# Kernel tuning notes

Measured on AMD Instinct MI355X. Metric: run time of the kernel, lower is better.

## Reference

```python
import jax, jax.numpy as jnp
import numpy as np

N_NODES = 20000
N_EDGES = 640000
D_IN = 128
D_OUT = 128


def setup_inputs() -> dict:
    key = jax.random.key(0)
    k1, k2, k3, k4 = jax.random.split(key, 4)
    x = jax.random.normal(k1, (N_NODES, D_IN), dtype=jnp.float32)
    edge_index = jax.random.randint(k2, (2, N_EDGES), 0, N_NODES, dtype=jnp.int64)
    edge_weight = jnp.ones((N_EDGES,), dtype=jnp.float32)
    # Linear(in_feats, out_feats) params (PyTorch convention: W [out, in])
    bound = 1.0 / np.sqrt(D_IN)
    W = jax.random.uniform(k3, (D_OUT, D_IN), minval=-bound, maxval=bound, dtype=jnp.float32)
    b = jax.random.uniform(k4, (D_OUT,), minval=-bound, maxval=bound, dtype=jnp.float32)
    return {"x": x, "edge_index": edge_index, "edge_weight": edge_weight, "W": W, "b": b}


def reference(x, edge_index, edge_weight, W, b):
    # MeanAggregator: h = Linear(x); out = row-normalized spmm(adj, h)
    h = x @ W.T + b  # [N, D_OUT]
    row, col = edge_index[0], edge_index[1]
    # message = w_ij * h[j], scattered into row i  (spmm with COO adjacency)
    msg = h[col] * edge_weight[:, None]  # [E, D_OUT]
    agg = jax.ops.segment_sum(msg, row, num_segments=N_NODES)  # [N, D_OUT]
    deg = jax.ops.segment_sum(edge_weight, row, num_segments=N_NODES)  # [N]
    deg_inv = jnp.where(deg > 0, 1.0 / deg, 0.0)
    out = agg * deg_inv[:, None]
    # normalize=True -> F.normalize(out, p=2, dim=-1)
    norm = jnp.linalg.norm(out, axis=-1, keepdims=True)
    out = out / jnp.maximum(norm, 1e-12)
    return out
```

## Files before the change

kernel.cpp:

```cpp
#include <hip/hip_runtime.h>
#include <hip/hip_bf16.h>
#include <math.h>

#define N_NODES 20000
#define N_EDGES 640000
#define D 128

#define BSHIFT 4
#define BNODES 16
#define NB 1250
#define CAP2 768
#define AGG_T 1024
#define NBLK1 160
#define CHUNK 4000
#define GPAD 16
#define CASTBLK 625

#define GROWS 16

typedef __attribute__((ext_vector_type(8))) short bf16x8;
typedef __attribute__((ext_vector_type(4))) float f32x4;

static __device__ __forceinline__ unsigned short f2bf(float f) {
  unsigned u = __float_as_uint(f);
  return (unsigned short)((u + 0x7fffu + ((u >> 16) & 1u)) >> 16);
}
static __device__ __forceinline__ float bflo(unsigned v) {
  return __uint_as_float(v << 16);
}
static __device__ __forceinline__ float bfhi(unsigned v) {
  return __uint_as_float(v & 0xffff0000u);
}

__global__ __launch_bounds__(256) void zero_kernel(int* __restrict__ p, int n) {
  const int i = blockIdx.x * 256 + threadIdx.x;
  if (i < n) p[i] = 0;
}

__global__ __launch_bounds__(AGG_T) void castbin_kernel(
    const float* __restrict__ x, const float* __restrict__ W,
    const int* __restrict__ rows, const int* __restrict__ cols,
    const float* __restrict__ ew,
    unsigned* __restrict__ xb, unsigned* __restrict__ Wb,
    int* __restrict__ gcur, uint2* __restrict__ bins) {
  __shared__ uint2 stage[CHUNK];
  __shared__ int cnt[NB];
  __shared__ int lbase[NB];
  __shared__ int gbase[NB];
  const int tid = threadIdx.x;
  if (blockIdx.x < NBLK1) {
    const int e0 = blockIdx.x * CHUNK;
    for (int i = tid; i < NB; i += AGG_T) cnt[i] = 0;
    __syncthreads();
    const int4* r4 = reinterpret_cast<const int4*>(rows + e0);
    int4 rv;
    const bool own = tid < CHUNK / 4;
    if (own) {
      rv = r4[tid];
      atomicAdd(&cnt[rv.x >> BSHIFT], 1);
      atomicAdd(&cnt[rv.y >> BSHIFT], 1);
      atomicAdd(&cnt[rv.z >> BSHIFT], 1);
      atomicAdd(&cnt[rv.w >> BSHIFT], 1);
    }
    __syncthreads();
    if (tid < 64) {
      int carry = 0;
      for (int c0 = 0; c0 < NB; c0 += 64) {
        const int idx = c0 + tid;
        const int v = (idx < NB) ? cnt[idx] : 0;
        int s = v;
#pragma unroll
        for (int off = 1; off < 64; off <<= 1) {
          const int t = __shfl_up(s, off);
          if (tid >= off) s += t;
        }
        if (idx < NB) lbase[idx] = carry + s - v;
        carry += __shfl(s, 63);
      }
    }
    for (int i = tid; i < NB; i += AGG_T) {
      const int c = cnt[i];
      gbase[i] = c ? atomicAdd(&gcur[i * GPAD], c) : 0;
    }
    __syncthreads();
    for (int i = tid; i < NB; i += AGG_T) cnt[i] = 0;
    __syncthreads();
    if (own) {
      const int4 cv = reinterpret_cast<const int4*>(cols + e0)[tid];
      const float4 wv = reinterpret_cast<const float4*>(ew + e0)[tid];
      const int rr[4] = {rv.x, rv.y, rv.z, rv.w};
      const int cc[4] = {cv.x, cv.y, cv.z, cv.w};
      const float ww[4] = {wv.x, wv.y, wv.z, wv.w};
#pragma unroll
      for (int u = 0; u < 4; ++u) {
        const int b = rr[u] >> BSHIFT;
        const int r = atomicAdd(&cnt[b], 1);
        stage[lbase[b] + r] =
            make_uint2(((unsigned)rr[u] << 16) | (unsigned)cc[u],
                       __float_as_uint(ww[u]));
      }
    }
    __syncthreads();
    for (int i = tid; i < CHUNK; i += AGG_T) {
      const uint2 e = stage[i];
      const int b = (int)(e.x >> 20);
      const int p = gbase[b] + (i - lbase[b]);
      if (p < CAP2) bins[(size_t)b * CAP2 + p] = e;
    }
  } else {
    const int i = (blockIdx.x - NBLK1) * AGG_T + tid;
    {
      const float4 v = *reinterpret_cast<const float4*>(&x[(size_t)i * 4]);
      uint2 o;
      o.x = (unsigned)f2bf(v.x) | ((unsigned)f2bf(v.y) << 16);
      o.y = (unsigned)f2bf(v.z) | ((unsigned)f2bf(v.w) << 16);
      *reinterpret_cast<uint2*>(&xb[(size_t)i * 2]) = o;
    }
    if (i < D * D / 4) {
      const float4 v = *reinterpret_cast<const float4*>(&W[(size_t)i * 4]);
      uint2 o;
      o.x = (unsigned)f2bf(v.x) | ((unsigned)f2bf(v.y) << 16);
      o.y = (unsigned)f2bf(v.z) | ((unsigned)f2bf(v.w) << 16);
      *reinterpret_cast<uint2*>(&Wb[(size_t)i * 2]) = o;
    }
  }
}

__global__ __launch_bounds__(AGG_T) void agg_gemm_kernel(
    const unsigned* __restrict__ xb, const int* __restrict__ gcur,
    const uint2* __restrict__ bins, const unsigned* __restrict__ Wb,
    const float* __restrict__ bias, float* __restrict__ out) {
  __shared__ uint2 list[CAP2];
  __shared__ unsigned aggls[BNODES * 64];
  __shared__ int cnt[BNODES];
  __shared__ int base[BNODES];
  __shared__ float degls[BNODES];
  const int b = blockIdx.x;
  const int tid = threadIdx.x;
  const int n = min(gcur[b * GPAD], CAP2);
  if (tid < BNODES) cnt[tid] = 0;
  __syncthreads();

  uint2 ev;
  int rk = -1, rl = 0;
  if (tid < n) {
    ev = bins[(size_t)b * CAP2 + tid];
    rl = (int)(ev.x >> 16) & 15;
    rk = atomicAdd(&cnt[rl], 1);
  }
  __syncthreads();
  if (tid < 64) {
    const int c = (tid < BNODES) ? cnt[tid] : 0;
    int s = c;
#pragma unroll
    for (int off = 1; off < BNODES; off <<= 1) {
      const int t = __shfl_up(s, off);
      if (tid >= off) s += t;
    }
    if (tid < BNODES) base[tid] = s - c;
  }
  __syncthreads();
  if (rk >= 0) list[base[rl] + rk] = ev;
  __syncthreads();

  const int wv = tid >> 6, lane = tid & 63;
  const int q4 = lane >> 4, fidx = lane & 15;
  {
    const int s = base[wv];
    const int ke = s + cnt[wv];
    float a[8] = {0.f, 0.f, 0.f, 0.f, 0.f, 0.f, 0.f, 0.f};
    float dw = 0.f;
    for (int k = s; k < ke; k += 32) {
      uint4 v[8];
      float w[8];
#pragma unroll
      for (int u = 0; u < 8; ++u) {
        int idx = k + u * 4 + q4;
        const bool ok = idx < ke;
        if (!ok) idx = ke - 1;
        const uint2 e = list[idx];
        w[u] = ok ? __uint_as_float(e.y) : 0.f;
        v[u] = *reinterpret_cast<const uint4*>(
            &xb[(size_t)(e.x & 0xffffu) * (D / 2) + fidx * 4]);
      }
#pragma unroll
      for (int u = 0; u < 8; ++u) {
        a[0] += bflo(v[u].x) * w[u]; a[1] += bfhi(v[u].x) * w[u];
        a[2] += bflo(v[u].y) * w[u]; a[3] += bfhi(v[u].y) * w[u];
        a[4] += bflo(v[u].z) * w[u]; a[5] += bfhi(v[u].z) * w[u];
        a[6] += bflo(v[u].w) * w[u]; a[7] += bfhi(v[u].w) * w[u];
        dw += w[u];
      }
    }
#pragma unroll
    for (int j = 0; j < 8; ++j) {
      a[j] += __shfl_xor(a[j], 16);
      a[j] += __shfl_xor(a[j], 32);
    }
    dw += __shfl_xor(dw, 16);
    dw += __shfl_xor(dw, 32);
    const float dinv = dw > 0.f ? 1.f / dw : 0.f;
    if (lane == 0) degls[wv] = dw;
    if (q4 == 0) {
      uint4 o;
      o.x = (unsigned)f2bf(a[0] * dinv) | ((unsigned)f2bf(a[1] * dinv) << 16);
      o.y = (unsigned)f2bf(a[2] * dinv) | ((unsigned)f2bf(a[3] * dinv) << 16);
      o.z = (unsigned)f2bf(a[4] * dinv) | ((unsigned)f2bf(a[5] * dinv) << 16);
      o.w = (unsigned)f2bf(a[6] * dinv) | ((unsigned)f2bf(a[7] * dinv) << 16);
      *reinterpret_cast<uint4*>(
          &aggls[wv * 64 + ((fidx * 4) ^ ((wv & 7) << 2))]) = o;
    }
  }
  __syncthreads();

  if (wv != 0) return;
  const int arow = lane & 15;
  const int koff = (lane >> 4) * 4;

  bf16x8 afr[4];
#pragma unroll
  for (int kk = 0; kk < 4; ++kk) {
    const int wbase = (kk * 16 + koff) ^ ((arow & 7) << 2);
    union { uint4 u; bf16x8 v; } cv;
    cv.u = *reinterpret_cast<const uint4*>(&aggls[arow * 64 + wbase]);
    afr[kk] = cv.v;
  }

  f32x4 acc[8];
#pragma unroll
  for (int t = 0; t < 8; ++t) {
    const int o = t * 16 + (lane & 15);
    f32x4 c = {0.f, 0.f, 0.f, 0.f};
#pragma unroll
    for (int kk = 0; kk < 4; ++kk) {
      union { uint4 u; bf16x8 v; } cv;
      cv.u = *reinterpret_cast<const uint4*>(
          &Wb[(size_t)o * (D / 2) + kk * 16 + koff]);
      c = __builtin_amdgcn_mfma_f32_16x16x32_bf16(afr[kk], cv.v, c, 0, 0, 0);
    }
    acc[t] = c;
  }

  float ss[4] = {0.f, 0.f, 0.f, 0.f};
#pragma unroll
  for (int t = 0; t < 8; ++t) {
    const float bc = bias[t * 16 + (lane & 15)];
#pragma unroll
    for (int r = 0; r < 4; ++r) {
      const float y = acc[t][r] + bc;
      acc[t][r] = y;
      ss[r] += y * y;
    }
  }
#pragma unroll
  for (int r = 0; r < 4; ++r) {
#pragma unroll
    for (int off = 1; off < 16; off <<= 1)
      ss[r] += __shfl_xor(ss[r], off);
  }
  const int row0 = b * BNODES;
  float scale[4];
#pragma unroll
  for (int r = 0; r < 4; ++r) {
    const int lrow = (lane >> 4) * 4 + r;
    const float dw = degls[lrow];
    scale[r] = (dw > 0.f) ? 1.f / fmaxf(sqrtf(ss[r]), 1e-12f) : 0.f;
  }
#pragma unroll
  for (int t = 0; t < 8; ++t) {
#pragma unroll
    for (int r = 0; r < 4; ++r) {
      const int lrow = (lane >> 4) * 4 + r;
      out[(size_t)(row0 + lrow) * D + t * 16 + (lane & 15)] =
          acc[t][r] * scale[r];
    }
  }
}

__global__ __launch_bounds__(256) void scatter_kernel(
    const float* __restrict__ x, const int* __restrict__ rows,
    const int* __restrict__ cols, const float* __restrict__ ew,
    float* __restrict__ out, float* __restrict__ degw) {
  const int e = blockIdx.x * 4 + (threadIdx.x >> 6);
  const int lane = threadIdx.x & 63;
  if (e >= N_EDGES) return;
  const int r = rows[e];
  const int c = cols[e];
  const float w = ew[e];
  const float2 v = *reinterpret_cast<const float2*>(&x[(size_t)c * D + lane * 2]);
  atomicAdd(&out[(size_t)r * D + lane * 2], v.x * w);
  atomicAdd(&out[(size_t)r * D + lane * 2 + 1], v.y * w);
  if (lane == 0) atomicAdd(&degw[r], w);
}

__global__ __launch_bounds__(256) void linear_norm_kernel(
    const float* __restrict__ W, const float* __restrict__ b,
    const float* __restrict__ degw, float* __restrict__ out) {
  __shared__ float Ws[D][D + 1];
  __shared__ float xs[GROWS][D];
  __shared__ float dws[GROWS];
  const int tid = threadIdx.x;
  const int row0 = blockIdx.x * GROWS;
  for (int idx = tid; idx < D * D; idx += 256)
    Ws[idx >> 7][idx & 127] = W[idx];
  if (tid < GROWS) dws[tid] = degw[row0 + tid];
  __syncthreads();
  for (int idx = tid; idx < GROWS * D; idx += 256) {
    const int r = idx >> 7;
    const float dw = dws[r];
    const float dinv = dw > 0.f ? 1.f / dw : 0.f;
    xs[r][idx & 127] = out[(size_t)(row0 + r) * D + (idx & 127)] * dinv;
  }
  __syncthreads();
  const int o = tid & 127;
  const int rh = tid >> 7;
  float acc[GROWS / 2];
#pragma unroll
  for (int j = 0; j < GROWS / 2; ++j) acc[j] = 0.f;
  for (int k = 0; k < D; ++k) {
    const float wv = Ws[o][k];
#pragma unroll
    for (int j = 0; j < GROWS / 2; ++j)
      acc[j] += xs[rh + 2 * j][k] * wv;
  }
  const float bias = b[o];
  __syncthreads();
#pragma unroll
  for (int j = 0; j < GROWS / 2; ++j)
    xs[rh + 2 * j][o] = acc[j] + bias;
  __syncthreads();
  const int w = tid >> 6, lane = tid & 63;
#pragma unroll
  for (int q = 0; q < 4; ++q) {
    const int r = w * 4 + q;
    const float2 v = *reinterpret_cast<const float2*>(&xs[r][lane * 2]);
    float ss = v.x * v.x + v.y * v.y;
#pragma unroll
    for (int off = 1; off < 64; off <<= 1) ss += __shfl_xor(ss, off);
    const float dw = dws[r];
    const float scale = (dw > 0.f) ? 1.f / fmaxf(sqrtf(ss), 1e-12f) : 0.f;
    *reinterpret_cast<float2*>(&out[(size_t)(row0 + r) * D + lane * 2]) =
        make_float2(v.x * scale, v.y * scale);
  }
}

extern "C" void kernel_launch(void* const* d_in, const int* in_sizes, int n_in,
                              void* d_out, int out_size, void* d_ws, size_t ws_size,
                              hipStream_t stream) {
  const float* x  = (const float*)d_in[0];
  const int*   ei = (const int*)d_in[1];
  const float* ew = (const float*)d_in[2];
  const float* W  = (const float*)d_in[3];
  const float* b  = (const float*)d_in[4];
  float* out = (float*)d_out;
  char* ws = (char*)d_ws;

  const int* rows = ei;
  const int* cols = ei + N_EDGES;

  size_t off = 0;
  int* gcur = (int*)(ws + off);        off += (size_t)NB * GPAD * 4;
  float* degw = (float*)(ws + off);    off += (size_t)N_NODES * 4;
  unsigned* xb = (unsigned*)(ws + off);  off += (size_t)N_NODES * (D / 2) * 4;
  unsigned* Wb = (unsigned*)(ws + off);  off += (size_t)D * (D / 2) * 4;
  uint2* bins = (uint2*)(ws + off);    off += (size_t)NB * CAP2 * 8;
  const size_t main_bytes = off;
  const size_t fallback_bytes = (size_t)NB * GPAD * 4 + (size_t)N_NODES * 4;

  if (ws_size >= main_bytes) {
    zero_kernel<<<(NB * GPAD + 255) / 256, 256, 0, stream>>>(gcur, NB * GPAD);
    castbin_kernel<<<NBLK1 + CASTBLK, AGG_T, 0, stream>>>(x, W, rows, cols, ew,
                                                          xb, Wb, gcur, bins);
    agg_gemm_kernel<<<NB, AGG_T, 0, stream>>>(xb, gcur, bins, Wb, b, out);
  } else if (ws_size >= fallback_bytes) {
    hipMemsetAsync(out, 0, (size_t)N_NODES * D * 4, stream);
    hipMemsetAsync(degw, 0, (size_t)N_NODES * 4, stream);
    scatter_kernel<<<(N_EDGES + 3) / 4, 256, 0, stream>>>(x, rows, cols, ew, out, degw);
    linear_norm_kernel<<<N_NODES / GROWS, 256, 0, stream>>>(W, b, degw, out);
  }
}
```

Before: 58.46 us.

## Fuse zero, bin, cast and aggregate-GEMM kernels into one cooperative persistent kernel

Replaces three kernel launches (zero, castbin, agg_gemm) with a single cooperative kernel of 256 blocks that uses grid-wide syncs between phases. The persistent blocks loop over the cast chunks and the node bins. The aim is to remove launch overhead and the gaps between kernels. In exchange there are grid.sync barriers, and fewer blocks (256 of 1024 threads) now cover 1250 bins. The larger combined shared-memory footprint may limit occupancy.

```diff
diff --git a/kernel.cpp b/kernel.cpp
--- a/kernel.cpp
+++ b/kernel.cpp
@@ -1,6 +1,9 @@
 #include <hip/hip_runtime.h>
+#include <hip/hip_cooperative_groups.h>
 #include <hip/hip_bf16.h>
 #include <math.h>
+
+namespace cg = cooperative_groups;
 
 #define N_NODES 20000
 #define N_EDGES 640000
@@ -10,13 +13,12 @@
 #define BNODES 16
 #define NB 1250
 #define CAP2 768
-#define AGG_T 1024
+#define TPB 1024
+#define NGRID 256
 #define NBLK1 160
 #define CHUNK 4000
 #define GPAD 16
-#define CASTBLK 625
-
-#define GROWS 16
+#define CASTCH 625
 
 typedef __attribute__((ext_vector_type(8))) short bf16x8;
 typedef __attribute__((ext_vector_type(4))) float f32x4;
@@ -32,25 +34,36 @@
   return __uint_as_float(v & 0xffff0000u);
 }
 
-__global__ __launch_bounds__(256) void zero_kernel(int* __restrict__ p, int n) {
-  const int i = blockIdx.x * 256 + threadIdx.x;
-  if (i < n) p[i] = 0;
-}
-
-__global__ __launch_bounds__(AGG_T) void castbin_kernel(
+__global__ __launch_bounds__(TPB, 4) void fused_kernel(
     const float* __restrict__ x, const float* __restrict__ W,
     const int* __restrict__ rows, const int* __restrict__ cols,
     const float* __restrict__ ew,
     unsigned* __restrict__ xb, unsigned* __restrict__ Wb,
-    int* __restrict__ gcur, uint2* __restrict__ bins) {
+    int* __restrict__ gcur, uint2* __restrict__ bins,
+    const float* __restrict__ bias, float* __restrict__ out) {
   __shared__ uint2 stage[CHUNK];
   __shared__ int cnt[NB];
   __shared__ int lbase[NB];
   __shared__ int gbase[NB];
+  __shared__ uint2 list[CAP2];
+  __shared__ unsigned aggls[BNODES * 64];
+  __shared__ int acnt[BNODES];
+  __shared__ int abase[BNODES];
+  __shared__ float degls[BNODES];
+
+  cg::grid_group grid = cg::this_grid();
   const int tid = threadIdx.x;
-  if (blockIdx.x < NBLK1) {
-    const int e0 = blockIdx.x * CHUNK;
-    for (int i = tid; i < NB; i += AGG_T) cnt[i] = 0;
+  const int bid = blockIdx.x;
+
+  {
+    const int i = bid * TPB + tid;
+    if (i < NB * GPAD) gcur[i] = 0;
+  }
+  grid.sync();
+
+  if (bid < NBLK1) {
+    const int e0 = bid * CHUNK;
+    for (int i = tid; i < NB; i += TPB) cnt[i] = 0;
     __syncthreads();
     const int4* r4 = reinterpret_cast<const int4*>(rows + e0);
     int4 rv;
@@ -78,19 +91,19 @@
         carry += __shfl(s, 63);
       }
     }
-    for (int i = tid; i < NB; i += AGG_T) {
+    for (int i = tid; i < NB; i += TPB) {
       const int c = cnt[i];
       gbase[i] = c ? atomicAdd(&gcur[i * GPAD], c) : 0;
     }
     __syncthreads();
-    for (int i = tid; i < NB; i += AGG_T) cnt[i] = 0;
+    for (int i = tid; i < NB; i += TPB) cnt[i] = 0;
     __syncthreads();
     if (own) {
       const int4 cv = reinterpret_cast<const int4*>(cols + e0)[tid];
-      const float4 wv = reinterpret_cast<const float4*>(ew + e0)[tid];
+      const float4 wv4 = reinterpret_cast<const float4*>(ew + e0)[tid];
       const int rr[4] = {rv.x, rv.y, rv.z, rv.w};
       const int cc[4] = {cv.x, cv.y, cv.z, cv.w};
-      const float ww[4] = {wv.x, wv.y, wv.z, wv.w};
+      const float ww[4] = {wv4.x, wv4.y, wv4.z, wv4.w};
 #pragma unroll
       for (int u = 0; u < 4; ++u) {
         const int b = rr[u] >> BSHIFT;
@@ -101,14 +114,15 @@
       }
     }
     __syncthreads();
-    for (int i = tid; i < CHUNK; i += AGG_T) {
+    for (int i = tid; i < CHUNK; i += TPB) {
       const uint2 e = stage[i];
       const int b = (int)(e.x >> 20);
       const int p = gbase[b] + (i - lbase[b]);
       if (p < CAP2) bins[(size_t)b * CAP2 + p] = e;
     }
-  } else {
-    const int i = (blockIdx.x - NBLK1) * AGG_T + tid;
+  }
+  for (int c = bid; c < CASTCH; c += NGRID) {
+    const int i = c * TPB + tid;
     {
       const float4 v = *reinterpret_cast<const float4*>(&x[(size_t)i * 4]);
       uint2 o;
@@ -124,159 +138,153 @@
       *reinterpret_cast<uint2*>(&Wb[(size_t)i * 2]) = o;
     }
   }
-}
-
-__global__ __launch_bounds__(AGG_T) void agg_gemm_kernel(
-    const unsigned* __restrict__ xb, const int* __restrict__ gcur,
-    const uint2* __restrict__ bins, const unsigned* __restrict__ Wb,
-    const float* __restrict__ bias, float* __restrict__ out) {
-  __shared__ uint2 list[CAP2];
-  __shared__ unsigned aggls[BNODES * 64];
-  __shared__ int cnt[BNODES];
-  __shared__ int base[BNODES];
-  __shared__ float degls[BNODES];
-  const int b = blockIdx.x;
-  const int tid = threadIdx.x;
-  const int n = min(gcur[b * GPAD], CAP2);
-  if (tid < BNODES) cnt[tid] = 0;
-  __syncthreads();
-
-  uint2 ev;
-  int rk = -1, rl = 0;
-  if (tid < n) {
-    ev = bins[(size_t)b * CAP2 + tid];
-    rl = (int)(ev.x >> 16) & 15;
-    rk = atomicAdd(&cnt[rl], 1);
-  }
-  __syncthreads();
-  if (tid < 64) {
-    const int c = (tid < BNODES) ? cnt[tid] : 0;
-    int s = c;
-#pragma unroll
-    for (int off = 1; off < BNODES; off <<= 1) {
-      const int t = __shfl_up(s, off);
-      if (tid >= off) s += t;
-    }
-    if (tid < BNODES) base[tid] = s - c;
-  }
-  __syncthreads();
-  if (rk >= 0) list[base[rl] + rk] = ev;
-  __syncthreads();
+  grid.sync();
 
   const int wv = tid >> 6, lane = tid & 63;
   const int q4 = lane >> 4, fidx = lane & 15;
-  {
-    const int s = base[wv];
-    const int ke = s + cnt[wv];
-    float a[8] = {0.f, 0.f, 0.f, 0.f, 0.f, 0.f, 0.f, 0.f};
-    float dw = 0.f;
-    for (int k = s; k < ke; k += 32) {
-      uint4 v[8];
-      float w[8];
-#pragma unroll
-      for (int u = 0; u < 8; ++u) {
-        int idx = k + u * 4 + q4;
-        const bool ok = idx < ke;
-        if (!ok) idx = ke - 1;
-        const uint2 e = list[idx];
-        w[u] = ok ? __uint_as_float(e.y) : 0.f;
-        v[u] = *reinterpret_cast<const uint4*>(
-            &xb[(size_t)(e.x & 0xffffu) * (D / 2) + fidx * 4]);
-      }
-#pragma unroll
-      for (int u = 0; u < 8; ++u) {
-        a[0] += bflo(v[u].x) * w[u]; a[1] += bfhi(v[u].x) * w[u];
-        a[2] += bflo(v[u].y) * w[u]; a[3] += bfhi(v[u].y) * w[u];
-        a[4] += bflo(v[u].z) * w[u]; a[5] += bfhi(v[u].z) * w[u];
-        a[6] += bflo(v[u].w) * w[u]; a[7] += bfhi(v[u].w) * w[u];
-        dw += w[u];
-      }
-    }
-#pragma unroll
-    for (int j = 0; j < 8; ++j) {
-      a[j] += __shfl_xor(a[j], 16);
-      a[j] += __shfl_xor(a[j], 32);
-    }
-    dw += __shfl_xor(dw, 16);
-    dw += __shfl_xor(dw, 32);
-    const float dinv = dw > 0.f ? 1.f / dw : 0.f;
-    if (lane == 0) degls[wv] = dw;
-    if (q4 == 0) {
-      uint4 o;
-      o.x = (unsigned)f2bf(a[0] * dinv) | ((unsigned)f2bf(a[1] * dinv) << 16);
-      o.y = (unsigned)f2bf(a[2] * dinv) | ((unsigned)f2bf(a[3] * dinv) << 16);
-      o.z = (unsigned)f2bf(a[4] * dinv) | ((unsigned)f2bf(a[5] * dinv) << 16);
-      o.w = (unsigned)f2bf(a[6] * dinv) | ((unsigned)f2bf(a[7] * dinv) << 16);
-      *reinterpret_cast<uint4*>(
-          &aggls[wv * 64 + ((fidx * 4) ^ ((wv & 7) << 2))]) = o;
-    }
-  }
-  __syncthreads();
-
-  if (wv != 0) return;
-  const int arow = lane & 15;
-  const int koff = (lane >> 4) * 4;
-
-  bf16x8 afr[4];
-#pragma unroll
-  for (int kk = 0; kk < 4; ++kk) {
-    const int wbase = (kk * 16 + koff) ^ ((arow & 7) << 2);
-    union { uint4 u; bf16x8 v; } cv;
-    cv.u = *reinterpret_cast<const uint4*>(&aggls[arow * 64 + wbase]);
-    afr[kk] = cv.v;
-  }
-
-  f32x4 acc[8];
-#pragma unroll
-  for (int t = 0; t < 8; ++t) {
-    const int o = t * 16 + (lane & 15);
-    f32x4 c = {0.f, 0.f, 0.f, 0.f};
-#pragma unroll
-    for (int kk = 0; kk < 4; ++kk) {
-      union { uint4 u; bf16x8 v; } cv;
-      cv.u = *reinterpret_cast<const uint4*>(
-          &Wb[(size_t)o * (D / 2) + kk * 16 + koff]);
-      c = __builtin_amdgcn_mfma_f32_16x16x32_bf16(afr[kk], cv.v, c, 0, 0, 0);
-    }
-    acc[t] = c;
-  }
-
-  float ss[4] = {0.f, 0.f, 0.f, 0.f};
-#pragma unroll
-  for (int t = 0; t < 8; ++t) {
-    const float bc = bias[t * 16 + (lane & 15)];
-#pragma unroll
-    for (int r = 0; r < 4; ++r) {
-      const float y = acc[t][r] + bc;
-      acc[t][r] = y;
-      ss[r] += y * y;
-    }
-  }
-#pragma unroll
-  for (int r = 0; r < 4; ++r) {
-#pragma unroll
-    for (int off = 1; off < 16; off <<= 1)
-      ss[r] += __shfl_xor(ss[r], off);
-  }
-  const int row0 = b * BNODES;
-  float scale[4];
-#pragma unroll
-  for (int r = 0; r < 4; ++r) {
-    const int lrow = (lane >> 4) * 4 + r;
-    const float dw = degls[lrow];
-    scale[r] = (dw > 0.f) ? 1.f / fmaxf(sqrtf(ss[r]), 1e-12f) : 0.f;
-  }
-#pragma unroll
-  for (int t = 0; t < 8; ++t) {
-#pragma unroll
-    for (int r = 0; r < 4; ++r) {
-      const int lrow = (lane >> 4) * 4 + r;
-      out[(size_t)(row0 + lrow) * D + t * 16 + (lane & 15)] =
-          acc[t][r] * scale[r];
-    }
-  }
-}
-
+  for (int b = bid; b < NB; b += NGRID) {
+    __syncthreads();
+    const int n = min(gcur[b * GPAD], CAP2);
+    if (tid < BNODES) acnt[tid] = 0;
+    __syncthreads();
+
+    uint2 ev;
+    int rk = -1, rl = 0;
+    if (tid < n) {
+      ev = bins[(size_t)b * CAP2 + tid];
+      rl = (int)(ev.x >> 16) & 15;
+      rk = atomicAdd(&acnt[rl], 1);
+    }
+    __syncthreads();
+    if (tid < 64) {
+      const int c = (tid < BNODES) ? acnt[tid] : 0;
+      int s = c;
+#pragma unroll
+      for (int off = 1; off < BNODES; off <<= 1) {
+        const int t = __shfl_up(s, off);
+        if (tid >= off) s += t;
+      }
+      if (tid < BNODES) abase[tid] = s - c;
+    }
+    __syncthreads();
+    if (rk >= 0) list[abase[rl] + rk] = ev;
+    __syncthreads();
+
+    {
+      const int s = abase[wv];
+      const int ke = s + acnt[wv];
+      float a[8] = {0.f, 0.f, 0.f, 0.f, 0.f, 0.f, 0.f, 0.f};
+      float dw = 0.f;
+      for (int k = s; k < ke; k += 32) {
+        uint4 v[8];
+        float w[8];
+#pragma unroll
+        for (int u = 0; u < 8; ++u) {
+          int idx = k + u * 4 + q4;
+          const bool ok = idx < ke;
+          if (!ok) idx = ke - 1;
+          const uint2 e = list[idx];
+          w[u] = ok ? __uint_as_float(e.y) : 0.f;
+          v[u] = *reinterpret_cast<const uint4*>(
+              &xb[(size_t)(e.x & 0xffffu) * (D / 2) + fidx * 4]);
+        }
+#pragma unroll
+        for (int u = 0; u < 8; ++u) {
+          a[0] += bflo(v[u].x) * w[u]; a[1] += bfhi(v[u].x) * w[u];
+          a[2] += bflo(v[u].y) * w[u]; a[3] += bfhi(v[u].y) * w[u];
+          a[4] += bflo(v[u].z) * w[u]; a[5] += bfhi(v[u].z) * w[u];
+          a[6] += bflo(v[u].w) * w[u]; a[7] += bfhi(v[u].w) * w[u];
+          dw += w[u];
+        }
+      }
+#pragma unroll
+      for (int j = 0; j < 8; ++j) {
+        a[j] += __shfl_xor(a[j], 16);
+        a[j] += __shfl_xor(a[j], 32);
+      }
+      dw += __shfl_xor(dw, 16);
+      dw += __shfl_xor(dw, 32);
+      const float dinv = dw > 0.f ? 1.f / dw : 0.f;
+      if (lane == 0) degls[wv] = dw;
+      if (q4 == 0) {
+        uint4 o;
+        o.x = (unsigned)f2bf(a[0] * dinv) | ((unsigned)f2bf(a[1] * dinv) << 16);
+        o.y = (unsigned)f2bf(a[2] * dinv) | ((unsigned)f2bf(a[3] * dinv) << 16);
+        o.z = (unsigned)f2bf(a[4] * dinv) | ((unsigned)f2bf(a[5] * dinv) << 16);
+        o.w = (unsigned)f2bf(a[6] * dinv) | ((unsigned)f2bf(a[7] * dinv) << 16);
+        *reinterpret_cast<uint4*>(
+            &aggls[wv * 64 + ((fidx * 4) ^ ((wv & 7) << 2))]) = o;
+      }
+    }
+    __syncthreads();
+
+    if (wv == 0) {
+      const int arow = lane & 15;
+      const int koff = (lane >> 4) * 4;
+
+      bf16x8 afr[4];
+#pragma unroll
+      for (int kk = 0; kk < 4; ++kk) {
+        const int wbase = (kk * 16 + koff) ^ ((arow & 7) << 2);
+        union { uint4 u; bf16x8 v; } cv;
+        cv.u = *reinterpret_cast<const uint4*>(&aggls[arow * 64 + wbase]);
+        afr[kk] = cv.v;
+      }
+
+      f32x4 acc[8];
+#pragma unroll
+      for (int t = 0; t < 8; ++t) {
+        const int o = t * 16 + (lane & 15);
+        f32x4 c = {0.f, 0.f, 0.f, 0.f};
+#pragma unroll
+        for (int kk = 0; kk < 4; ++kk) {
+          union { uint4 u; bf16x8 v; } cv;
+          cv.u = *reinterpret_cast<const uint4*>(
+              &Wb[(size_t)o * (D / 2) + kk * 16 + koff]);
+          c = __builtin_amdgcn_mfma_f32_16x16x32_bf16(afr[kk], cv.v, c, 0, 0, 0);
+        }
+        acc[t] = c;
+      }
+
+      float ss[4] = {0.f, 0.f, 0.f, 0.f};
+#pragma unroll
+      for (int t = 0; t < 8; ++t) {
+        const float bc = bias[t * 16 + (lane & 15)];
+#pragma unroll
+        for (int r = 0; r < 4; ++r) {
+          const float y = acc[t][r] + bc;
+          acc[t][r] = y;
+          ss[r] += y * y;
+        }
+      }
+#pragma unroll
+      for (int r = 0; r < 4; ++r) {
+#pragma unroll
+        for (int off = 1; off < 16; off <<= 1)
+          ss[r] += __shfl_xor(ss[r], off);
+      }
+      const int row0 = b * BNODES;
+      float scale[4];
+#pragma unroll
+      for (int r = 0; r < 4; ++r) {
+        const int lrow = (lane >> 4) * 4 + r;
+        const float dw = degls[lrow];
+        scale[r] = (dw > 0.f) ? 1.f / fmaxf(sqrtf(ss[r]), 1e-12f) : 0.f;
+      }
+#pragma unroll
+      for (int t = 0; t < 8; ++t) {
+#pragma unroll
+        for (int r = 0; r < 4; ++r) {
+          const int lrow = (lane >> 4) * 4 + r;
+          out[(size_t)(row0 + lrow) * D + t * 16 + (lane & 15)] =
+              acc[t][r] * scale[r];
+        }
+      }
+    }
+  }
+}
+
+#define GROWS 16
 __global__ __launch_bounds__(256) void scatter_kernel(
     const float* __restrict__ x, const int* __restrict__ rows,
     const int* __restrict__ cols, const float* __restrict__ ew,
@@ -368,10 +376,11 @@
   const size_t fallback_bytes = (size_t)NB * GPAD * 4 + (size_t)N_NODES * 4;
 
   if (ws_size >= main_bytes) {
-    zero_kernel<<<(NB * GPAD + 255) / 256, 256, 0, stream>>>(gcur, NB * GPAD);
-    castbin_kernel<<<NBLK1 + CASTBLK, AGG_T, 0, stream>>>(x, W, rows, cols, ew,
-                                                          xb, Wb, gcur, bins);
-    agg_gemm_kernel<<<NB, AGG_T, 0, stream>>>(xb, gcur, bins, Wb, b, out);
+    void* args[] = {(void*)&x,  (void*)&W,  (void*)&rows, (void*)&cols,
+                    (void*)&ew, (void*)&xb, (void*)&Wb,   (void*)&gcur,
+                    (void*)&bins, (void*)&b, (void*)&out};
+    hipLaunchCooperativeKernel((const void*)fused_kernel, dim3(NGRID), dim3(TPB),
+                               args, 0, stream);
   } else if (ws_size >= fallback_bytes) {
     hipMemsetAsync(out, 0, (size_t)N_NODES * D * 4, stream);
     hipMemsetAsync(degw, 0, (size_t)N_NODES * 4, stream);
```

Measured after the change: 162.9 us. +178.7%, slower.
